# Kernel optimization log

Hardware: AMD Instinct MI355X
Metric: run time of the kernel (lower is better)

Reference implementation:

```python
import jax, jax.numpy as jnp
import numpy as np

DIM = 1024
HEADS = 16
HEAD_DIM = DIM // HEADS
SEQ = 2048
BATCH = 2


def setup_inputs() -> dict:
    key = jax.random.key(0)
    ks = jax.random.split(key, 9)
    s = 1.0 / np.sqrt(DIM)
    mk = lambda k: jax.random.uniform(k, (DIM, DIM), jnp.float32, -s, s)
    mb = lambda k: jax.random.uniform(k, (DIM,), jnp.float32, -s, s)
    return {
        "x": jax.random.normal(ks[0], (BATCH, SEQ, DIM), jnp.float32),
        "wq": mk(ks[1]), "bq": mb(ks[2]),
        "wk": mk(ks[3]), "bk": mb(ks[4]),
        "wv": mk(ks[5]), "bv": mb(ks[6]),
        "wo": mk(ks[7]), "bo": mb(ks[8]),
    }


def reference(x, wq, bq, wk, bk, wv, bv, wo, bo):
    b, s, d = x.shape
    inv_sqrt_hd = 1.0 / np.sqrt(HEAD_DIM)
    # torch Linear: y = x @ W.T + b
    q = (x @ wq.T + bq).reshape(b, s, HEADS, HEAD_DIM)
    k = (x @ wk.T + bk).reshape(b, s, HEADS, HEAD_DIM)
    v = (x @ wv.T + bv).reshape(b, s, HEADS, HEAD_DIM)
    # scores [b, h, s, s]; NOTE: original forward never applies the causal mask buffer
    scores = jnp.einsum("bqhd,bkhd->bhqk", q, k) * inv_sqrt_hd
    a = jax.nn.softmax(scores, axis=-1)
    o = jnp.einsum("bhqk,bkhd->bqhd", a, v).reshape(b, s, d)
    o = o @ wo.T + bo
    return (o, a.mean(axis=1))
```

## Files before the change

kernel.cpp:

```cpp
#include <hip/hip_runtime.h>
#include <stdint.h>

#define DIMD 1024
#define HEADS 16
#define HD 64
#define SEQ 2048
#define BATCH 2
#define MTOT (BATCH*SEQ)

typedef __attribute__((ext_vector_type(4))) float f32x4;
typedef __attribute__((ext_vector_type(8))) short bf16x8;
typedef __attribute__((ext_vector_type(8))) unsigned short ushort8;
typedef __attribute__((ext_vector_type(4))) unsigned short usx4;

#define GL_LDS16(gp, lp) __builtin_amdgcn_global_load_lds( \
    (const __attribute__((address_space(1))) unsigned int*)(gp), \
    (__attribute__((address_space(3))) unsigned int*)(lp), 16, 0, 0)

__device__ __forceinline__ unsigned short f2bf(float f) {
    unsigned int u = __builtin_bit_cast(unsigned int, f);
    u = (u + 0x7FFFu + ((u >> 16) & 1u)) >> 16;
    return (unsigned short)u;
}
__device__ __forceinline__ float bf2f(unsigned short s) {
    unsigned int u = ((unsigned int)s) << 16;
    return __builtin_bit_cast(float, u);
}

__global__ __launch_bounds__(256) void cvt_f32_bf16(const float* __restrict__ in,
                                                    unsigned short* __restrict__ out, int n) {
    int i = (blockIdx.x * 256 + threadIdx.x) * 8;
    if (i >= n) return;
    f32x4 a = *(const f32x4*)(in + i);
    f32x4 b = *(const f32x4*)(in + i + 4);
    ushort8 o;
    o[0] = f2bf(a[0]); o[1] = f2bf(a[1]); o[2] = f2bf(a[2]); o[3] = f2bf(a[3]);
    o[4] = f2bf(b[0]); o[5] = f2bf(b[1]); o[6] = f2bf(b[2]); o[7] = f2bf(b[3]);
    *(ushort8*)(out + i) = o;
}

__global__ __launch_bounds__(256) void cvt_w4(const float* __restrict__ w0, const float* __restrict__ w1,
                                              const float* __restrict__ w2, const float* __restrict__ w3,
                                              unsigned short* __restrict__ dst) {
    const int sel = blockIdx.x >> 9;
    const float* src = sel == 0 ? w0 : sel == 1 ? w1 : sel == 2 ? w2 : w3;
    int i = ((blockIdx.x & 511) * 256 + threadIdx.x) * 8;
    f32x4 a = *(const f32x4*)(src + i);
    f32x4 b = *(const f32x4*)(src + i + 4);
    ushort8 o;
    o[0] = f2bf(a[0]); o[1] = f2bf(a[1]); o[2] = f2bf(a[2]); o[3] = f2bf(a[3]);
    o[4] = f2bf(b[0]); o[5] = f2bf(b[1]); o[6] = f2bf(b[2]); o[7] = f2bf(b[3]);
    *(ushort8*)(dst + (size_t)sel * 1048576 + i) = o;
}

template<bool F32OUT>
__global__ __launch_bounds__(256, 2) void gemm_lds(const unsigned short* __restrict__ X,
                                                   const unsigned short* __restrict__ W,
                                                   const float* __restrict__ bias,
                                                   void* __restrict__ outp,
                                                   int Nv, int Kv) {
    __shared__ unsigned short As[2][128 * 64];
    __shared__ unsigned short Bs[2][64 * 64];
    const int tid = threadIdx.x, wid = tid >> 6;
    const int lane = tid & 63, lr = lane & 15, hi = lane >> 4;
    const int m0 = blockIdx.y * 128;
    const int n0 = blockIdx.x * 64;
    const int mq = (wid >> 1) * 64, nq = (wid & 1) * 32;
    const int NT = Kv >> 6;

    f32x4 acc[4][2];
    #pragma unroll
    for (int i = 0; i < 4; ++i)
        #pragma unroll
        for (int j = 0; j < 2; ++j) acc[i][j] = (f32x4){0.f, 0.f, 0.f, 0.f};

    #pragma unroll
    for (int it = 0; it < 4; ++it) {
        int li = it * 256 + tid, row = li >> 3, seg = li & 7;
        GL_LDS16(X + (size_t)(m0 + row) * Kv + ((seg ^ (row & 7)) << 3), &As[0][li * 8]);
    }
    #pragma unroll
    for (int it = 0; it < 2; ++it) {
        int li = it * 256 + tid, row = li >> 3, seg = li & 7;
        GL_LDS16(W + (size_t)(n0 + row) * Kv + ((seg ^ (row & 7)) << 3), &Bs[0][li * 8]);
    }
    __syncthreads();

    #pragma unroll 2
    for (int t = 0; t < NT; ++t) {
        const int cur = t & 1, nxt = cur ^ 1;
        if (t + 1 < NT) {
            const int k1 = (t + 1) << 6;
            #pragma unroll
            for (int it = 0; it < 4; ++it) {
                int li = it * 256 + tid, row = li >> 3, seg = li & 7;
                GL_LDS16(X + (size_t)(m0 + row) * Kv + k1 + ((seg ^ (row & 7)) << 3),
                         &As[nxt][li * 8]);
            }
            #pragma unroll
            for (int it = 0; it < 2; ++it) {
                int li = it * 256 + tid, row = li >> 3, seg = li & 7;
                GL_LDS16(W + (size_t)(n0 + row) * Kv + k1 + ((seg ^ (row & 7)) << 3),
                         &Bs[nxt][li * 8]);
            }
        }
        #pragma unroll
        for (int kk = 0; kk < 2; ++kk) {
            bf16x8 af[4], bfr[2];
            #pragma unroll
            for (int i = 0; i < 4; ++i) {
                int row = mq + 16 * i + lr;
                int seg = (kk * 4 + hi) ^ (row & 7);
                af[i] = *(const bf16x8*)(&As[cur][row * 64 + seg * 8]);
            }
            #pragma unroll
            for (int j = 0; j < 2; ++j) {
                int row = nq + 16 * j + lr;
                int seg = (kk * 4 + hi) ^ (row & 7);
                bfr[j] = *(const bf16x8*)(&Bs[cur][row * 64 + seg * 8]);
            }
            #pragma unroll
            for (int i = 0; i < 4; ++i)
                #pragma unroll
                for (int j = 0; j < 2; ++j)
                    acc[i][j] = __builtin_amdgcn_mfma_f32_16x16x32_bf16(af[i], bfr[j], acc[i][j], 0, 0, 0);
        }
        __syncthreads();
    }

    #pragma unroll
    for (int j = 0; j < 2; ++j) {
        const int col = n0 + nq + 16 * j + lr;
        const float bv = bias[col];
        #pragma unroll
        for (int i = 0; i < 4; ++i) {
            #pragma unroll
            for (int r = 0; r < 4; ++r) {
                const int row = m0 + mq + 16 * i + 4 * hi + r;
                float v = acc[i][j][r] + bv;
                if (F32OUT) ((float*)outp)[(size_t)row * Nv + col] = v;
                else        ((unsigned short*)outp)[(size_t)row * Nv + col] = f2bf(v);
            }
        }
    }
}

__global__ __launch_bounds__(256) void transpose_v(const unsigned short* __restrict__ v,
                                                   unsigned short* __restrict__ vT) {
    __shared__ unsigned short tile[64][72];
    const int bh = blockIdx.y;
    const int b = bh >> 4, h = bh & 15;
    const int s0 = blockIdx.x * 64;
    const int t = threadIdx.x;
    #pragma unroll
    for (int it = 0; it < 2; ++it) {
        int li = it * 256 + t;
        int row = li >> 3, c8 = (li & 7) * 8;
        ushort8 val = *(const ushort8*)(v + (size_t)(b * SEQ + s0 + row) * DIMD + h * HD + c8);
        *(ushort8*)&tile[row][c8] = val;
    }
    __syncthreads();
    #pragma unroll
    for (int it = 0; it < 2; ++it) {
        int li = it * 256 + t;
        int d = li >> 3, s8 = (li & 7) * 8;
        ushort8 o;
        #pragma unroll
        for (int j = 0; j < 8; ++j) o[j] = tile[s8 + j][d];
        *(ushort8*)(vT + (size_t)(bh * HD + d) * SEQ + s0 + s8) = o;
    }
}

__global__ __launch_bounds__(256, 4) void score_pv_kernel(const unsigned short* __restrict__ Q,
                                                          const unsigned short* __restrict__ Kt,
                                                          const unsigned short* __restrict__ vT,
                                                          unsigned short* __restrict__ Eb,
                                                          float* __restrict__ rlb,
                                                          unsigned short* __restrict__ attn, int b) {
    __shared__ unsigned short Ks[2][64 * 64];
    __shared__ unsigned short Vs[2][64 * 64];
    __shared__ unsigned short Es[32 * 68];
    __shared__ float ps[4][2][16];
    __shared__ float rls[32];
    const int tid = threadIdx.x, wid = tid >> 6, lane = tid & 63;
    const int lr = lane & 15, hi = lane >> 4;
    const int h = blockIdx.y;
    const int q0 = blockIdx.x * 32;
    const unsigned short* Kbase = Kt + (size_t)b * SEQ * DIMD + h * HD;
    const unsigned short* Vbase = vT + (size_t)(b * HEADS + h) * HD * SEQ;

    const unsigned short* qbase = Q + (size_t)(b * SEQ + q0) * DIMD + h * HD + 8 * hi;
    bf16x8 qb0[2], qb1[2];
    #pragma unroll
    for (int s = 0; s < 2; ++s) {
        const unsigned short* qp = qbase + (size_t)(16 * s + lr) * DIMD;
        qb0[s] = *(const bf16x8*)qp;
        qb1[s] = *(const bf16x8*)(qp + 32);
    }

    #pragma unroll
    for (int it = 0; it < 2; ++it) {
        int li = it * 256 + tid, row = li >> 3, seg = li & 7;
        GL_LDS16(Kbase + (size_t)row * DIMD + ((seg ^ (row & 7)) << 3), &Ks[0][li * 8]);
    }
    #pragma unroll
    for (int it = 0; it < 2; ++it) {
        int li = it * 256 + tid, row = li >> 3, seg = li & 7;
        GL_LDS16(Vbase + (size_t)row * SEQ + ((seg ^ (row & 7)) << 3), &Vs[0][li * 8]);
    }
    __syncthreads();

    float lsum[2] = {0.f, 0.f};
    f32x4 oacc[2];
    oacc[0] = (f32x4){0.f, 0.f, 0.f, 0.f};
    oacc[1] = (f32x4){0.f, 0.f, 0.f, 0.f};
    const int mq = (wid >> 1) * 16;
    const int nd = (wid & 1) * 32;
    const int erow = tid >> 3, ecol = (tid & 7) * 8;

    for (int t = 0; t < 32; ++t) {
        const int cur = t & 1, nxt = cur ^ 1;
        if (t + 1 < 32) {
            const int kb1 = (t + 1) * 64;
            #pragma unroll
            for (int it = 0; it < 2; ++it) {
                int li = it * 256 + tid, row = li >> 3, seg = li & 7;
                GL_LDS16(Kbase + (size_t)(kb1 + row) * DIMD + ((seg ^ (row & 7)) << 3),
                         &Ks[nxt][li * 8]);
            }
            #pragma unroll
            for (int it = 0; it < 2; ++it) {
                int li = it * 256 + tid, row = li >> 3, seg = li & 7;
                GL_LDS16(Vbase + (size_t)row * SEQ + kb1 + ((seg ^ (row & 7)) << 3),
                         &Vs[nxt][li * 8]);
            }
        }
        const int krow = wid * 16 + lr;
        bf16x8 a0 = *(const bf16x8*)(&Ks[cur][krow * 64 + ((hi       ^ (krow & 7)) << 3)]);
        bf16x8 a1 = *(const bf16x8*)(&Ks[cur][krow * 64 + (((4 + hi) ^ (krow & 7)) << 3)]);
        #pragma unroll
        for (int s = 0; s < 2; ++s) {
            f32x4 acc = (f32x4){0.f, 0.f, 0.f, 0.f};
            acc = __builtin_amdgcn_mfma_f32_16x16x32_bf16(a0, qb0[s], acc, 0, 0, 0);
            acc = __builtin_amdgcn_mfma_f32_16x16x32_bf16(a1, qb1[s], acc, 0, 0, 0);
            float e0 = __expf(acc[0] * 0.125f);
            float e1 = __expf(acc[1] * 0.125f);
            float e2 = __expf(acc[2] * 0.125f);
            float e3 = __expf(acc[3] * 0.125f);
            lsum[s] += (e0 + e1) + (e2 + e3);
            usx4 pk;
            pk[0] = f2bf(e0); pk[1] = f2bf(e1); pk[2] = f2bf(e2); pk[3] = f2bf(e3);
            *(usx4*)(&Es[(16 * s + lr) * 68 + wid * 16 + 4 * hi]) = pk;
        }
        __syncthreads();

        ushort8 ev = *(const ushort8*)(&Es[erow * 68 + ecol]);
        *(ushort8*)(Eb + ((size_t)h * SEQ + q0 + erow) * SEQ + t * 64 + ecol) = ev;

        #pragma unroll
        for (int kk = 0; kk < 2; ++kk) {
            bf16x8 ea = *(const bf16x8*)(&Es[(mq + lr) * 68 + kk * 32 + 8 * hi]);
            #pragma unroll
            for (int j = 0; j < 2; ++j) {
                int vrow = nd + 16 * j + lr;
                int seg = (kk * 4 + hi) ^ (vrow & 7);
                bf16x8 vb = *(const bf16x8*)(&Vs[cur][vrow * 64 + seg * 8]);
                oacc[j] = __builtin_amdgcn_mfma_f32_16x16x32_bf16(ea, vb, oacc[j], 0, 0, 0);
            }
        }
        __syncthreads();
    }

    #pragma unroll
    for (int s = 0; s < 2; ++s) {
        float l = lsum[s];
        l += __shfl_xor(l, 16);
        l += __shfl_xor(l, 32);
        if (lane < 16) ps[wid][s][lane] = l;
    }
    __syncthreads();
    if (tid < 32) {
        int s = tid >> 4, qq = tid & 15;
        float tot = ps[0][s][qq] + ps[1][s][qq] + ps[2][s][qq] + ps[3][s][qq];
        float r = 1.0f / tot;
        rlb[h * SEQ + q0 + 16 * s + qq] = r;
        rls[16 * s + qq] = r;
    }
    __syncthreads();

    #pragma unroll
    for (int r = 0; r < 4; ++r) {
        const int ql = mq + 4 * hi + r;
        const float rv = rls[ql];
        #pragma unroll
        for (int j = 0; j < 2; ++j)
            attn[(size_t)(b * SEQ + q0 + ql) * DIMD + h * HD + nd + 16 * j + lr] =
                f2bf(oacc[j][r] * rv);
    }
}

__global__ __launch_bounds__(256) void mean2_kernel(const unsigned short* __restrict__ Eb,
                                                    const float* __restrict__ rlb,
                                                    float* __restrict__ out1b) {
    __shared__ float rls[16];
    const int q = blockIdx.x, t = threadIdx.x;
    if (t < 16) rls[t] = rlb[t * SEQ + q] * 0.0625f;
    __syncthreads();
    const int k0 = t * 8;
    float acc[8] = {0.f, 0.f, 0.f, 0.f, 0.f, 0.f, 0.f, 0.f};
    #pragma unroll
    for (int h = 0; h < HEADS; ++h) {
        ushort8 e = *(const ushort8*)(Eb + ((size_t)h * SEQ + q) * SEQ + k0);
        float rv = rls[h];
        #pragma unroll
        for (int j = 0; j < 8; ++j) acc[j] += bf2f(e[j]) * rv;
    }
    f32x4 o0 = (f32x4){acc[0], acc[1], acc[2], acc[3]};
    f32x4 o1 = (f32x4){acc[4], acc[5], acc[6], acc[7]};
    *(f32x4*)(out1b + (size_t)q * SEQ + k0) = o0;
    *(f32x4*)(out1b + (size_t)q * SEQ + k0 + 4) = o1;
}

extern "C" void kernel_launch(void* const* d_in, const int* in_sizes, int n_in,
                              void* d_out, int out_size, void* d_ws, size_t ws_size,
                              hipStream_t stream) {
    const float* x  = (const float*)d_in[0];
    const float* wq = (const float*)d_in[1];
    const float* bq = (const float*)d_in[2];
    const float* wk = (const float*)d_in[3];
    const float* bk = (const float*)d_in[4];
    const float* wv = (const float*)d_in[5];
    const float* bv = (const float*)d_in[6];
    const float* wo = (const float*)d_in[7];
    const float* bo = (const float*)d_in[8];

    float* o_out    = (float*)d_out;
    float* mean_out = o_out + 4194304;

    unsigned short* xb   = (unsigned short*)d_ws;
    unsigned short* wqb  = xb   + 4194304;
    unsigned short* wkb  = wqb  + 1048576;
    unsigned short* wvb  = wkb  + 1048576;
    unsigned short* wob  = wvb  + 1048576;
    unsigned short* qb   = wob  + 1048576;
    unsigned short* kb   = qb   + 4194304;
    unsigned short* vTb  = kb   + 4194304;
    unsigned short* attb = vTb  + 4194304;
    float*          rlb  = (float*)(attb + 4194304);
    unsigned short* Eb   = (unsigned short*)(rlb + 65536);
    unsigned short* vb   = Eb;

    cvt_f32_bf16<<<2048, 256, 0, stream>>>(x, xb, 4194304);
    cvt_w4<<<2048, 256, 0, stream>>>(wq, wk, wv, wo, wqb);

    gemm_lds<false><<<dim3(16, 32), 256, 0, stream>>>(xb, wqb, bq, qb, DIMD, DIMD);
    gemm_lds<false><<<dim3(16, 32), 256, 0, stream>>>(xb, wkb, bk, kb, DIMD, DIMD);
    gemm_lds<false><<<dim3(16, 32), 256, 0, stream>>>(xb, wvb, bv, vb, DIMD, DIMD);
    transpose_v<<<dim3(32, 32), 256, 0, stream>>>(vb, vTb);

    for (int b = 0; b < BATCH; ++b) {
        float* rl_b = rlb + b * HEADS * SEQ;
        score_pv_kernel<<<dim3(64, 16), 256, 0, stream>>>(qb, kb, vTb, Eb, rl_b, attb, b);
        mean2_kernel<<<2048, 256, 0, stream>>>(Eb, rl_b, mean_out + (size_t)b * SEQ * SEQ);
    }

    gemm_lds<true><<<dim3(16, 32), 256, 0, stream>>>(attb, wob, bo, o_out, DIMD, DIMD);
}
```

Baseline: 224.3 us.

## Fuse QKV GEMMs into one launch and enlarge attention and mean tiles

Merges the three Q/K/V projection GEMM launches into one grid of 48x32 blocks that selects weight, bias and output per block, which cuts launch overhead and tail effects. The score/PV kernel now handles 64 queries per block instead of 32, so each K/V tile loaded into LDS is reused across twice as many queries, at the cost of more registers and LDS and lower occupancy (launch bounds 4 to 2). The head-mean kernel processes two query rows per block with 16 elements per thread. Fewer, larger blocks may hurt load balance.

Result: faster. 207.8 us (-7.3%).

```diff
diff --git a/kernel.cpp b/kernel.cpp
--- a/kernel.cpp
+++ b/kernel.cpp
@@ -54,6 +54,96 @@
 }
 
 template<bool F32OUT>
+__device__ __forceinline__ void gemm_body(const unsigned short* __restrict__ X,
+                                          const unsigned short* __restrict__ W,
+                                          const float* __restrict__ bias,
+                                          void* __restrict__ outp,
+                                          int m0, int n0, int Nv, int Kv,
+                                          unsigned short (*As)[128 * 64],
+                                          unsigned short (*Bs)[64 * 64]) {
+    const int tid = threadIdx.x, wid = tid >> 6;
+    const int lane = tid & 63, lr = lane & 15, hi = lane >> 4;
+    const int mq = (wid >> 1) * 64, nq = (wid & 1) * 32;
+    const int NT = Kv >> 6;
+
+    f32x4 acc[4][2];
+    #pragma unroll
+    for (int i = 0; i < 4; ++i)
+        #pragma unroll
+        for (int j = 0; j < 2; ++j) acc[i][j] = (f32x4){0.f, 0.f, 0.f, 0.f};
+
+    #pragma unroll
+    for (int it = 0; it < 4; ++it) {
+        int li = it * 256 + tid, row = li >> 3, seg = li & 7;
+        GL_LDS16(X + (size_t)(m0 + row) * Kv + ((seg ^ (row & 7)) << 3), &As[0][li * 8]);
+    }
+    #pragma unroll
+    for (int it = 0; it < 2; ++it) {
+        int li = it * 256 + tid, row = li >> 3, seg = li & 7;
+        GL_LDS16(W + (size_t)(n0 + row) * Kv + ((seg ^ (row & 7)) << 3), &Bs[0][li * 8]);
+    }
+    __syncthreads();
+
+    #pragma unroll 2
+    for (int t = 0; t < NT; ++t) {
+        const int cur = t & 1, nxt = cur ^ 1;
+        if (t + 1 < NT) {
+            const int k1 = (t + 1) << 6;
+            #pragma unroll
+            for (int it = 0; it < 4; ++it) {
+                int li = it * 256 + tid, row = li >> 3, seg = li & 7;
+                GL_LDS16(X + (size_t)(m0 + row) * Kv + k1 + ((seg ^ (row & 7)) << 3),
+                         &As[nxt][li * 8]);
+            }
+            #pragma unroll
+            for (int it = 0; it < 2; ++it) {
+                int li = it * 256 + tid, row = li >> 3, seg = li & 7;
+                GL_LDS16(W + (size_t)(n0 + row) * Kv + k1 + ((seg ^ (row & 7)) << 3),
+                         &Bs[nxt][li * 8]);
+            }
+        }
+        #pragma unroll
+        for (int kk = 0; kk < 2; ++kk) {
+            bf16x8 af[4], bfr[2];
+            #pragma unroll
+            for (int i = 0; i < 4; ++i) {
+                int row = mq + 16 * i + lr;
+                int seg = (kk * 4 + hi) ^ (row & 7);
+                af[i] = *(const bf16x8*)(&As[cur][row * 64 + seg * 8]);
+            }
+            #pragma unroll
+            for (int j = 0; j < 2; ++j) {
+                int row = nq + 16 * j + lr;
+                int seg = (kk * 4 + hi) ^ (row & 7);
+                bfr[j] = *(const bf16x8*)(&Bs[cur][row * 64 + seg * 8]);
+            }
+            #pragma unroll
+            for (int i = 0; i < 4; ++i)
+                #pragma unroll
+                for (int j = 0; j < 2; ++j)
+                    acc[i][j] = __builtin_amdgcn_mfma_f32_16x16x32_bf16(af[i], bfr[j], acc[i][j], 0, 0, 0);
+        }
+        __syncthreads();
+    }
+
+    #pragma unroll
+    for (int j = 0; j < 2; ++j) {
+        const int col = n0 + nq + 16 * j + lr;
+        const float bv = bias[col];
+        #pragma unroll
+        for (int i = 0; i < 4; ++i) {
+            #pragma unroll
+            for (int r = 0; r < 4; ++r) {
+                const int row = m0 + mq + 16 * i + 4 * hi + r;
+                float v = acc[i][j][r] + bv;
+                if (F32OUT) ((float*)outp)[(size_t)row * Nv + col] = v;
+                else        ((unsigned short*)outp)[(size_t)row * Nv + col] = f2bf(v);
+            }
+        }
+    }
+}
+
+template<bool F32OUT>
 __global__ __launch_bounds__(256, 2) void gemm_lds(const unsigned short* __restrict__ X,
                                                    const unsigned short* __restrict__ W,
                                                    const float* __restrict__ bias,
@@ -61,88 +151,25 @@
                                                    int Nv, int Kv) {
     __shared__ unsigned short As[2][128 * 64];
     __shared__ unsigned short Bs[2][64 * 64];
-    const int tid = threadIdx.x, wid = tid >> 6;
-    const int lane = tid & 63, lr = lane & 15, hi = lane >> 4;
-    const int m0 = blockIdx.y * 128;
-    const int n0 = blockIdx.x * 64;
-    const int mq = (wid >> 1) * 64, nq = (wid & 1) * 32;
-    const int NT = Kv >> 6;
-
-    f32x4 acc[4][2];
-    #pragma unroll
-    for (int i = 0; i < 4; ++i)
-        #pragma unroll
-        for (int j = 0; j < 2; ++j) acc[i][j] = (f32x4){0.f, 0.f, 0.f, 0.f};
-
-    #pragma unroll
-    for (int it = 0; it < 4; ++it) {
-        int li = it * 256 + tid, row = li >> 3, seg = li & 7;
-        GL_LDS16(X + (size_t)(m0 + row) * Kv + ((seg ^ (row & 7)) << 3), &As[0][li * 8]);
-    }
-    #pragma unroll
-    for (int it = 0; it < 2; ++it) {
-        int li = it * 256 + tid, row = li >> 3, seg = li & 7;
-        GL_LDS16(W + (size_t)(n0 + row) * Kv + ((seg ^ (row & 7)) << 3), &Bs[0][li * 8]);
-    }
-    __syncthreads();
-
-    #pragma unroll 2
-    for (int t = 0; t < NT; ++t) {
-        const int cur = t & 1, nxt = cur ^ 1;
-        if (t + 1 < NT) {
-            const int k1 = (t + 1) << 6;
-            #pragma unroll
-            for (int it = 0; it < 4; ++it) {
-                int li = it * 256 + tid, row = li >> 3, seg = li & 7;
-                GL_LDS16(X + (size_t)(m0 + row) * Kv + k1 + ((seg ^ (row & 7)) << 3),
-                         &As[nxt][li * 8]);
-            }
-            #pragma unroll
-            for (int it = 0; it < 2; ++it) {
-                int li = it * 256 + tid, row = li >> 3, seg = li & 7;
-                GL_LDS16(W + (size_t)(n0 + row) * Kv + k1 + ((seg ^ (row & 7)) << 3),
-                         &Bs[nxt][li * 8]);
-            }
-        }
-        #pragma unroll
-        for (int kk = 0; kk < 2; ++kk) {
-            bf16x8 af[4], bfr[2];
-            #pragma unroll
-            for (int i = 0; i < 4; ++i) {
-                int row = mq + 16 * i + lr;
-                int seg = (kk * 4 + hi) ^ (row & 7);
-                af[i] = *(const bf16x8*)(&As[cur][row * 64 + seg * 8]);
-            }
-            #pragma unroll
-            for (int j = 0; j < 2; ++j) {
-                int row = nq + 16 * j + lr;
-                int seg = (kk * 4 + hi) ^ (row & 7);
-                bfr[j] = *(const bf16x8*)(&Bs[cur][row * 64 + seg * 8]);
-            }
-            #pragma unroll
-            for (int i = 0; i < 4; ++i)
-                #pragma unroll
-                for (int j = 0; j < 2; ++j)
-                    acc[i][j] = __builtin_amdgcn_mfma_f32_16x16x32_bf16(af[i], bfr[j], acc[i][j], 0, 0, 0);
-        }
-        __syncthreads();
-    }
-
-    #pragma unroll
-    for (int j = 0; j < 2; ++j) {
-        const int col = n0 + nq + 16 * j + lr;
-        const float bv = bias[col];
-        #pragma unroll
-        for (int i = 0; i < 4; ++i) {
-            #pragma unroll
-            for (int r = 0; r < 4; ++r) {
-                const int row = m0 + mq + 16 * i + 4 * hi + r;
-                float v = acc[i][j][r] + bv;
-                if (F32OUT) ((float*)outp)[(size_t)row * Nv + col] = v;
-                else        ((unsigned short*)outp)[(size_t)row * Nv + col] = f2bf(v);
-            }
-        }
-    }
+    gemm_body<F32OUT>(X, W, bias, outp, blockIdx.y * 128, blockIdx.x * 64, Nv, Kv, As, Bs);
+}
+
+__global__ __launch_bounds__(256, 2) void gemm_qkv(const unsigned short* __restrict__ X,
+                                                   const unsigned short* __restrict__ Wall,
+                                                   const float* __restrict__ b0,
+                                                   const float* __restrict__ b1,
+                                                   const float* __restrict__ b2,
+                                                   unsigned short* __restrict__ o0,
+                                                   unsigned short* __restrict__ o1,
+                                                   unsigned short* __restrict__ o2) {
+    __shared__ unsigned short As[2][128 * 64];
+    __shared__ unsigned short Bs[2][64 * 64];
+    const int sel = blockIdx.x >> 4;
+    const int n0 = (blockIdx.x & 15) * 64;
+    const unsigned short* W = Wall + (size_t)sel * 1048576;
+    const float* bias = sel == 0 ? b0 : sel == 1 ? b1 : b2;
+    unsigned short* out = sel == 0 ? o0 : sel == 1 ? o1 : o2;
+    gemm_body<false>(X, W, bias, out, blockIdx.y * 128, n0, DIMD, DIMD, As, Bs);
 }
 
 __global__ __launch_bounds__(256) void transpose_v(const unsigned short* __restrict__ v,
@@ -171,7 +198,7 @@
     }
 }
 
-__global__ __launch_bounds__(256, 4) void score_pv_kernel(const unsigned short* __restrict__ Q,
+__global__ __launch_bounds__(256, 2) void score_pv_kernel(const unsigned short* __restrict__ Q,
                                                           const unsigned short* __restrict__ Kt,
                                                           const unsigned short* __restrict__ vT,
                                                           unsigned short* __restrict__ Eb,
@@ -179,20 +206,20 @@
                                                           unsigned short* __restrict__ attn, int b) {
     __shared__ unsigned short Ks[2][64 * 64];
     __shared__ unsigned short Vs[2][64 * 64];
-    __shared__ unsigned short Es[32 * 68];
-    __shared__ float ps[4][2][16];
-    __shared__ float rls[32];
+    __shared__ unsigned short Es[64 * 68];
+    __shared__ float ps[4][4][16];
+    __shared__ float rls[64];
     const int tid = threadIdx.x, wid = tid >> 6, lane = tid & 63;
     const int lr = lane & 15, hi = lane >> 4;
     const int h = blockIdx.y;
-    const int q0 = blockIdx.x * 32;
+    const int q0 = blockIdx.x * 64;
     const unsigned short* Kbase = Kt + (size_t)b * SEQ * DIMD + h * HD;
     const unsigned short* Vbase = vT + (size_t)(b * HEADS + h) * HD * SEQ;
 
     const unsigned short* qbase = Q + (size_t)(b * SEQ + q0) * DIMD + h * HD + 8 * hi;
-    bf16x8 qb0[2], qb1[2];
-    #pragma unroll
-    for (int s = 0; s < 2; ++s) {
+    bf16x8 qb0[4], qb1[4];
+    #pragma unroll
+    for (int s = 0; s < 4; ++s) {
         const unsigned short* qp = qbase + (size_t)(16 * s + lr) * DIMD;
         qb0[s] = *(const bf16x8*)qp;
         qb1[s] = *(const bf16x8*)(qp + 32);
@@ -210,13 +237,14 @@
     }
     __syncthreads();
 
-    float lsum[2] = {0.f, 0.f};
-    f32x4 oacc[2];
-    oacc[0] = (f32x4){0.f, 0.f, 0.f, 0.f};
-    oacc[1] = (f32x4){0.f, 0.f, 0.f, 0.f};
-    const int mq = (wid >> 1) * 16;
+    float lsum[4] = {0.f, 0.f, 0.f, 0.f};
+    f32x4 oacc[2][2];
+    #pragma unroll
+    for (int i = 0; i < 2; ++i)
+        #pragma unroll
+        for (int j = 0; j < 2; ++j) oacc[i][j] = (f32x4){0.f, 0.f, 0.f, 0.f};
+    const int mq = (wid >> 1) * 32;
     const int nd = (wid & 1) * 32;
-    const int erow = tid >> 3, ecol = (tid & 7) * 8;
 
     for (int t = 0; t < 32; ++t) {
         const int cur = t & 1, nxt = cur ^ 1;
@@ -239,7 +267,7 @@
         bf16x8 a0 = *(const bf16x8*)(&Ks[cur][krow * 64 + ((hi       ^ (krow & 7)) << 3)]);
         bf16x8 a1 = *(const bf16x8*)(&Ks[cur][krow * 64 + (((4 + hi) ^ (krow & 7)) << 3)]);
         #pragma unroll
-        for (int s = 0; s < 2; ++s) {
+        for (int s = 0; s < 4; ++s) {
             f32x4 acc = (f32x4){0.f, 0.f, 0.f, 0.f};
             acc = __builtin_amdgcn_mfma_f32_16x16x32_bf16(a0, qb0[s], acc, 0, 0, 0);
             acc = __builtin_amdgcn_mfma_f32_16x16x32_bf16(a1, qb1[s], acc, 0, 0, 0);
@@ -254,32 +282,43 @@
         }
         __syncthreads();
 
-        ushort8 ev = *(const ushort8*)(&Es[erow * 68 + ecol]);
-        *(ushort8*)(Eb + ((size_t)h * SEQ + q0 + erow) * SEQ + t * 64 + ecol) = ev;
+        #pragma unroll
+        for (int it = 0; it < 2; ++it) {
+            int li = it * 256 + tid, row = li >> 3, col = (li & 7) * 8;
+            ushort8 ev = *(const ushort8*)(&Es[row * 68 + col]);
+            *(ushort8*)(Eb + ((size_t)h * SEQ + q0 + row) * SEQ + t * 64 + col) = ev;
+        }
 
         #pragma unroll
         for (int kk = 0; kk < 2; ++kk) {
-            bf16x8 ea = *(const bf16x8*)(&Es[(mq + lr) * 68 + kk * 32 + 8 * hi]);
+            bf16x8 ea[2], vb[2];
+            #pragma unroll
+            for (int i = 0; i < 2; ++i)
+                ea[i] = *(const bf16x8*)(&Es[(mq + 16 * i + lr) * 68 + kk * 32 + 8 * hi]);
             #pragma unroll
             for (int j = 0; j < 2; ++j) {
                 int vrow = nd + 16 * j + lr;
                 int seg = (kk * 4 + hi) ^ (vrow & 7);
-                bf16x8 vb = *(const bf16x8*)(&Vs[cur][vrow * 64 + seg * 8]);
-                oacc[j] = __builtin_amdgcn_mfma_f32_16x16x32_bf16(ea, vb, oacc[j], 0, 0, 0);
-            }
+                vb[j] = *(const bf16x8*)(&Vs[cur][vrow * 64 + seg * 8]);
+            }
+            #pragma unroll
+            for (int i = 0; i < 2; ++i)
+                #pragma unroll
+                for (int j = 0; j < 2; ++j)
+                    oacc[i][j] = __builtin_amdgcn_mfma_f32_16x16x32_bf16(ea[i], vb[j], oacc[i][j], 0, 0, 0);
         }
         __syncthreads();
     }
 
     #pragma unroll
-    for (int s = 0; s < 2; ++s) {
+    for (int s = 0; s < 4; ++s) {
         float l = lsum[s];
         l += __shfl_xor(l, 16);
         l += __shfl_xor(l, 32);
         if (lane < 16) ps[wid][s][lane] = l;
     }
     __syncthreads();
-    if (tid < 32) {
+    if (tid < 64) {
         int s = tid >> 4, qq = tid & 15;
         float tot = ps[0][s][qq] + ps[1][s][qq] + ps[2][s][qq] + ps[3][s][qq];
         float r = 1.0f / tot;
@@ -289,36 +328,46 @@
     __syncthreads();
 
     #pragma unroll
-    for (int r = 0; r < 4; ++r) {
-        const int ql = mq + 4 * hi + r;
-        const float rv = rls[ql];
-        #pragma unroll
-        for (int j = 0; j < 2; ++j)
-            attn[(size_t)(b * SEQ + q0 + ql) * DIMD + h * HD + nd + 16 * j + lr] =
-                f2bf(oacc[j][r] * rv);
+    for (int i = 0; i < 2; ++i) {
+        #pragma unroll
+        for (int r = 0; r < 4; ++r) {
+            const int ql = mq + 16 * i + 4 * hi + r;
+            const float rv = rls[ql];
+            #pragma unroll
+            for (int j = 0; j < 2; ++j)
+                attn[(size_t)(b * SEQ + q0 + ql) * DIMD + h * HD + nd + 16 * j + lr] =
+                    f2bf(oacc[i][j][r] * rv);
+        }
     }
 }
 
 __global__ __launch_bounds__(256) void mean2_kernel(const unsigned short* __restrict__ Eb,
                                                     const float* __restrict__ rlb,
                                                     float* __restrict__ out1b) {
-    __shared__ float rls[16];
-    const int q = blockIdx.x, t = threadIdx.x;
-    if (t < 16) rls[t] = rlb[t * SEQ + q] * 0.0625f;
-    __syncthreads();
-    const int k0 = t * 8;
-    float acc[8] = {0.f, 0.f, 0.f, 0.f, 0.f, 0.f, 0.f, 0.f};
+    __shared__ float rls[2][16];
+    const int q0 = blockIdx.x * 2, t = threadIdx.x;
+    if (t < 32) rls[t >> 4][t & 15] = rlb[(t & 15) * SEQ + q0 + (t >> 4)] * 0.0625f;
+    __syncthreads();
+    const int r = t >> 7, k0 = (t & 127) * 16;
+    const size_t qrow = (size_t)(q0 + r);
+    float acc[16];
+    #pragma unroll
+    for (int j = 0; j < 16; ++j) acc[j] = 0.f;
     #pragma unroll
     for (int h = 0; h < HEADS; ++h) {
-        ushort8 e = *(const ushort8*)(Eb + ((size_t)h * SEQ + q) * SEQ + k0);
-        float rv = rls[h];
-        #pragma unroll
-        for (int j = 0; j < 8; ++j) acc[j] += bf2f(e[j]) * rv;
-    }
-    f32x4 o0 = (f32x4){acc[0], acc[1], acc[2], acc[3]};
-    f32x4 o1 = (f32x4){acc[4], acc[5], acc[6], acc[7]};
-    *(f32x4*)(out1b + (size_t)q * SEQ + k0) = o0;
-    *(f32x4*)(out1b + (size_t)q * SEQ + k0 + 4) = o1;
+        const unsigned short* ep = Eb + ((size_t)h * SEQ + qrow) * SEQ + k0;
+        ushort8 e0 = *(const ushort8*)ep;
+        ushort8 e1 = *(const ushort8*)(ep + 8);
+        float rv = rls[r][h];
+        #pragma unroll
+        for (int j = 0; j < 8; ++j) acc[j]     += bf2f(e0[j]) * rv;
+        #pragma unroll
+        for (int j = 0; j < 8; ++j) acc[8 + j] += bf2f(e1[j]) * rv;
+    }
+    float* op = out1b + qrow * SEQ + k0;
+    #pragma unroll
+    for (int v = 0; v < 4; ++v)
+        *(f32x4*)(op + 4 * v) = (f32x4){acc[4*v], acc[4*v+1], acc[4*v+2], acc[4*v+3]};
 }
 
 extern "C" void kernel_launch(void* const* d_in, const int* in_sizes, int n_in,
@@ -353,15 +402,13 @@
     cvt_f32_bf16<<<2048, 256, 0, stream>>>(x, xb, 4194304);
     cvt_w4<<<2048, 256, 0, stream>>>(wq, wk, wv, wo, wqb);
 
-    gemm_lds<false><<<dim3(16, 32), 256, 0, stream>>>(xb, wqb, bq, qb, DIMD, DIMD);
-    gemm_lds<false><<<dim3(16, 32), 256, 0, stream>>>(xb, wkb, bk, kb, DIMD, DIMD);
-    gemm_lds<false><<<dim3(16, 32), 256, 0, stream>>>(xb, wvb, bv, vb, DIMD, DIMD);
+    gemm_qkv<<<dim3(48, 32), 256, 0, stream>>>(xb, wqb, bq, bk, bv, qb, kb, vb);
     transpose_v<<<dim3(32, 32), 256, 0, stream>>>(vb, vTb);
 
     for (int b = 0; b < BATCH; ++b) {
         float* rl_b = rlb + b * HEADS * SEQ;
-        score_pv_kernel<<<dim3(64, 16), 256, 0, stream>>>(qb, kb, vTb, Eb, rl_b, attb, b);
-        mean2_kernel<<<2048, 256, 0, stream>>>(Eb, rl_b, mean_out + (size_t)b * SEQ * SEQ);
+        score_pv_kernel<<<dim3(32, 16), 256, 0, stream>>>(qb, kb, vTb, Eb, rl_b, attb, b);
+        mean2_kernel<<<1024, 256, 0, stream>>>(Eb, rl_b, mean_out + (size_t)b * SEQ * SEQ);
     }
 
     gemm_lds<true><<<dim3(16, 32), 256, 0, stream>>>(attb, wob, bo, o_out, DIMD, DIMD);
```
